# Kernel optimization log

Measured on AMD Instinct MI355X. Metric: run time of the kernel, lower is better.

The kernel has to match this reference:

```python
import jax, jax.numpy as jnp
import numpy as np

N, E = 100000, 1600000
IN, HID, HEADS, OUT = 128, 16, 8, 40
NEG_SLOPE = 0.2


def setup_inputs() -> dict:
    key = jax.random.key(0)
    ks = jax.random.split(key, 10)
    glorot = lambda k, shape, fan: (jax.random.normal(k, shape, jnp.float32) / np.float32(np.sqrt(fan)))
    return {
        "x": jax.random.normal(ks[0], (N, IN), jnp.float32),
        "edge_index": jax.random.randint(ks[1], (2, E), 0, N, dtype=jnp.int64),
        "W1": glorot(ks[2], (IN, HEADS * HID), IN),
        "att_src1": glorot(ks[3], (HEADS, HID), HID),
        "att_dst1": glorot(ks[4], (HEADS, HID), HID),
        "b1": jnp.zeros((HEADS * HID,), jnp.float32),
        "W2": glorot(ks[5], (HEADS * HID, OUT), HEADS * HID),
        "att_src2": glorot(ks[6], (1, OUT), OUT),
        "att_dst2": glorot(ks[7], (1, OUT), OUT),
        "b2": jnp.zeros((OUT,), jnp.float32),
    }


def gat_conv(x, W, a_src, a_dst, b, src, dst, n, heads, ch, concat):
    # x: [n, in], W: [in, heads*ch]
    h = (x @ W).reshape(n, heads, ch)                      # [n, H, C]
    e_s = jnp.einsum("nhc,hc->nh", h, a_src)               # per-node src logits
    e_d = jnp.einsum("nhc,hc->nh", h, a_dst)               # per-node dst logits
    alpha = jax.nn.leaky_relu(e_s[src] + e_d[dst], NEG_SLOPE)  # [E, H]
    # numerically stable softmax over incoming edges of each dst node
    m = jax.lax.stop_gradient(jax.ops.segment_max(alpha, dst, num_segments=n))
    ex = jnp.exp(alpha - m[dst])
    denom = jax.ops.segment_sum(ex, dst, num_segments=n)
    a = ex / (denom[dst] + 1e-16)                          # [E, H]
    out = jax.ops.segment_sum(h[src] * a[:, :, None], dst, num_segments=n)  # [n, H, C]
    out = out.reshape(n, heads * ch) if concat else out.mean(axis=1)
    return out + b


def reference(x, edge_index, W1, att_src1, att_dst1, b1, W2, att_src2, att_dst2, b2):
    n = x.shape[0]
    loops = jnp.arange(n, dtype=edge_index.dtype)
    src = jnp.concatenate([edge_index[0], loops])  # add_self_loops (PyG default)
    dst = jnp.concatenate([edge_index[1], loops])
    h1 = jax.nn.relu(gat_conv(x, W1, att_src1, att_dst1, b1, src, dst, n, HEADS, HID, True))
    # F.dropout(training=False) is identity in inference
    h2 = gat_conv(h1, W2, att_src2, att_dst2, b2, src, dst, n, 1, OUT, False)
    return jax.nn.log_softmax(h2, axis=1)
```

## Files before the change

### kernel.cpp

```cpp
#include <hip/hip_runtime.h>
#include <hip/hip_fp16.h>
#include <math.h>

#define NN 100000
#define EE 1600000
#define ET (EE + NN)
#define BWN 64
#define NBUCK 1563
#define ACHUNK 4096
#define NAB 416
#define MAXS 1792

typedef _Float16 f16x8 __attribute__((ext_vector_type(8)));
typedef float f32x4 __attribute__((ext_vector_type(4)));
typedef float f32x2 __attribute__((ext_vector_type(2)));

__device__ __forceinline__ float lrelu(float x) { return x > 0.f ? x : 0.2f * x; }

__global__ void k_w1pack(const float* __restrict__ W1, __half* __restrict__ w1p) {
    int idx = blockIdx.x * 256 + threadIdx.x;
    int j = idx & 7, lane = (idx >> 3) & 63, k0 = (idx >> 9) & 3;
    int ct = (idx >> 11) & 7;
    int k = k0 * 32 + (lane >> 4) * 8 + j;
    int c = ct * 16 + (lane & 15);
    _Float16 v = (_Float16)W1[k * 128 + c];
    w1p[idx] = *(__half*)&v;
}

__global__ void k_w2pack(const float* __restrict__ W2, __half* __restrict__ w2p) {
    int idx = blockIdx.x * 256 + threadIdx.x;
    int j = idx & 7, lane = (idx >> 3) & 63, k0 = (idx >> 9) & 3;
    int ct = idx >> 11;
    int k = k0 * 32 + (lane >> 4) * 8 + j;
    int c = ct * 16 + (lane & 15);
    _Float16 v = (_Float16)((c < 40) ? W2[k * 40 + c] : 0.f);
    w2p[idx] = *(__half*)&v;
}

__global__ __launch_bounds__(256) void k_gemm1(
        const float* __restrict__ x, const __half* __restrict__ w1p,
        const float* __restrict__ as1, const float* __restrict__ ad1,
        unsigned* __restrict__ h1b, float* __restrict__ es1, float* __restrict__ ed1) {
    int tid = threadIdx.x;
    int w = tid >> 6, lane = tid & 63;
    int rb = blockIdx.x * 64 + w * 16;
    int l15 = lane & 15, rg = lane >> 4;

    int arow = rb + l15;
    bool aok = arow < NN;
    const float4* x4 = (const float4*)x;
    f16x8 ah[4];
    #pragma unroll
    for (int k0 = 0; k0 < 4; ++k0) {
        float4 p0 = make_float4(0.f, 0.f, 0.f, 0.f), p1 = p0;
        if (aok) {
            int fi = arow * 32 + k0 * 8 + rg * 2;
            p0 = x4[fi];
            p1 = x4[fi + 1];
        }
        float pv[8] = {p0.x, p0.y, p0.z, p0.w, p1.x, p1.y, p1.z, p1.w};
        #pragma unroll
        for (int j = 0; j < 8; ++j) ah[k0][j] = (_Float16)pv[j];
    }

    const f16x8* w1f = (const f16x8*)w1p;
    f32x4 acc[8];
    #pragma unroll
    for (int ct = 0; ct < 8; ++ct) acc[ct] = (f32x4){0.f, 0.f, 0.f, 0.f};
    #pragma unroll
    for (int ct = 0; ct < 8; ++ct) {
        #pragma unroll
        for (int k0 = 0; k0 < 4; ++k0) {
            f16x8 bh = w1f[(ct * 4 + k0) * 64 + lane];
            acc[ct] = __builtin_amdgcn_mfma_f32_16x16x32_f16(bh, ah[k0], acc[ct], 0, 0, 0);
        }
    }

    int row = rb + l15;
    bool rok = row < NN;
    #pragma unroll
    for (int ct = 0; ct < 8; ++ct) {
        if (rok) {
            unsigned pw = __builtin_amdgcn_cvt_pk_fp8_f32(acc[ct][0], acc[ct][1], 0u, false);
            pw = __builtin_amdgcn_cvt_pk_fp8_f32(acc[ct][2], acc[ct][3], pw, true);
            h1b[row * 32 + ct * 4 + rg] = pw;
        }
        float4 a4 = ((const float4*)as1)[ct * 4 + rg];
        float4 d4 = ((const float4*)ad1)[ct * 4 + rg];
        float s = acc[ct][0] * a4.x + acc[ct][1] * a4.y + acc[ct][2] * a4.z + acc[ct][3] * a4.w;
        float d = acc[ct][0] * d4.x + acc[ct][1] * d4.y + acc[ct][2] * d4.z + acc[ct][3] * d4.w;
        s += __shfl_xor(s, 16); s += __shfl_xor(s, 32);
        d += __shfl_xor(d, 16); d += __shfl_xor(d, 32);
        if (rg == 0 && rok) { es1[row * 8 + ct] = s; ed1[row * 8 + ct] = d; }
    }
}

__global__ void k_bhist(const int* __restrict__ dst, int* __restrict__ bcnt) {
    __shared__ int lh[NBUCK];
    int t = threadIdx.x;
    for (int i = t; i < NBUCK; i += 256) lh[i] = 0;
    __syncthreads();
    int c0 = blockIdx.x * ACHUNK;
    #pragma unroll
    for (int i = 0; i < 16; ++i) {
        int e = c0 + t + i * 256;
        if (e < ET) {
            int d = (e < EE) ? dst[e] : e - EE;
            atomicAdd(&lh[d >> 6], 1);
        }
    }
    __syncthreads();
    for (int i = t; i < NBUCK; i += 256) {
        int c = lh[i];
        if (c) atomicAdd(&bcnt[i], c);
    }
}

__global__ void k_bscan(const int* __restrict__ bcnt, int* __restrict__ bbase,
                        int* __restrict__ bcur) {
    __shared__ int sd[256];
    int t = threadIdx.x;
    int base = t * 8;
    int v[8];
    int s = 0;
    #pragma unroll
    for (int j = 0; j < 8; ++j) {
        int i = base + j;
        v[j] = (i < NBUCK) ? bcnt[i] : 0;
        s += v[j];
    }
    sd[t] = s;
    __syncthreads();
    for (int off = 1; off < 256; off <<= 1) {
        int x = (t >= off) ? sd[t - off] : 0;
        __syncthreads();
        sd[t] += x;
        __syncthreads();
    }
    int excl = sd[t] - s;
    #pragma unroll
    for (int j = 0; j < 8; ++j) {
        int i = base + j;
        if (i <= NBUCK) { bbase[i] = excl; if (i < NBUCK) bcur[i] = excl; }
        excl += v[j];
    }
}

__global__ void k_bscatter(const int* __restrict__ src, const int* __restrict__ dst,
                           int* __restrict__ bcur, unsigned int* __restrict__ bedge) {
    __shared__ int lh[NBUCK];
    __shared__ int lb[NBUCK];
    int t = threadIdx.x;
    for (int i = t; i < NBUCK; i += 256) lh[i] = 0;
    __syncthreads();
    int c0 = blockIdx.x * ACHUNK;
    unsigned int val[16];
    int bkt[16];
    int rnk[16];
    #pragma unroll
    for (int i = 0; i < 16; ++i) {
        int e = c0 + t + i * 256;
        if (e < ET) {
            int s, d;
            if (e < EE) { s = src[e]; d = dst[e]; } else { s = d = e - EE; }
            int b = d >> 6;
            bkt[i] = b;
            val[i] = (unsigned)s | ((unsigned)(d & 63) << 24);
            rnk[i] = atomicAdd(&lh[b], 1);
        } else bkt[i] = -1;
    }
    __syncthreads();
    for (int i = t; i < NBUCK; i += 256) {
        int c = lh[i];
        lb[i] = c ? atomicAdd(&bcur[i], c) : 0;
    }
    __syncthreads();
    #pragma unroll
    for (int i = 0; i < 16; ++i)
        if (bkt[i] >= 0) bedge[lb[bkt[i]] + rnk[i]] = val[i];
}

__global__ void k_place(const unsigned int* __restrict__ bedge,
                        const int* __restrict__ bbase, int* __restrict__ rp,
                        int* __restrict__ col) {
    __shared__ int lh[BWN];
    __shared__ int ex[BWN + 1];
    __shared__ int lcur[BWN];
    __shared__ int stg[MAXS];
    int b = blockIdx.x, t = threadIdx.x;
    int beg = bbase[b], end = bbase[b + 1];
    if (t < BWN) { lh[t] = 0; lcur[t] = 0; }
    __syncthreads();
    for (int e = beg + t; e < end; e += 256) atomicAdd(&lh[(bedge[e] >> 24) & 63], 1);
    __syncthreads();
    if (t < 64) {
        int v = lh[t];
        int x = v;
        #pragma unroll
        for (int off = 1; off < 64; off <<= 1) {
            int y = __shfl_up(x, off);
            if (t >= off) x += y;
        }
        ex[t] = x - v;
        if (t == 63) ex[64] = x;
    }
    __syncthreads();
    int n = b * BWN + t;
    if (t < BWN && n < NN) rp[n] = beg + ex[t];
    if (b == 0 && t == 0) rp[NN] = ET;
    int S = ex[BWN];
    int lane = t & 63, w = t >> 6;
    if (S <= MAXS) {
        for (int e = beg + t; e < end; e += 256) {
            unsigned u = bedge[e];
            int i = (u >> 24) & 63;
            int pos = ex[i] + atomicAdd(&lcur[i], 1);
            stg[pos] = (int)(u & 0xFFFFFFu);
        }
        __syncthreads();
        for (int i = w; i < BWN; i += 4) {
            int sb = ex[i], d = lh[i];
            if (d <= 1) continue;
            if (d <= 64) {
                int vv = (lane < d) ? stg[sb + lane] : 0x7fffffff;
                #pragma unroll
                for (int k = 2; k <= 64; k <<= 1) {
                    #pragma unroll
                    for (int j = k >> 1; j > 0; j >>= 1) {
                        int other = __shfl_xor(vv, j);
                        bool lower = (lane & j) == 0;
                        bool up = (lane & k) == 0;
                        vv = (lower == up) ? min(vv, other) : max(vv, other);
                    }
                }
                if (lane < d) stg[sb + lane] = vv;
            } else if (lane == 0) {
                for (int p = sb + 1; p < sb + d; ++p) {
                    int key = stg[p]; int j = p - 1;
                    while (j >= sb && stg[j] > key) { stg[j + 1] = stg[j]; --j; }
                    stg[j + 1] = key;
                }
            }
        }
        __syncthreads();
        for (int j = t; j < S; j += 256) col[beg + j] = stg[j];
    } else {
        for (int e = beg + t; e < end; e += 256) {
            unsigned u = bedge[e];
            int i = (u >> 24) & 63;
            int pos = beg + ex[i] + atomicAdd(&lcur[i], 1);
            col[pos] = (int)(u & 0xFFFFFFu);
        }
        __syncthreads();
        if (t < BWN) {
            int sb = beg + ex[t], d = lh[t];
            for (int p = sb + 1; p < sb + d; ++p) {
                int key = col[p]; int j = p - 1;
                while (j >= sb && col[j] > key) { col[j + 1] = col[j]; --j; }
                col[j + 1] = key;
            }
        }
    }
}

__global__ void k_agg1(const int* __restrict__ rp, const int* __restrict__ col,
                       const uint4* __restrict__ h1v, const float* __restrict__ es1,
                       const float* __restrict__ ed1, const float* __restrict__ b1,
                       __half* __restrict__ out1h) {
    int gid = blockIdx.x * blockDim.x + threadIdx.x;
    int n = gid >> 3;
    int l = threadIdx.x & 7;
    if (n >= NN) return;
    float edn = ed1[n * 8 + l];
    int beg = rp[n], end = rp[n + 1];
    float acc[16];
    #pragma unroll
    for (int j = 0; j < 16; ++j) acc[j] = 0.f;
    float den = 0.f;
    int e = beg;
    int sA = col[e];
    int eB = (e + 1 < end) ? e + 1 : e;
    int sB = col[eB];
    float esA = es1[sA * 8 + l], esB = es1[sB * 8 + l];
    uint4 uA = h1v[sA * 8 + l];
    uint4 uB = h1v[sB * 8 + l];
    while (e < end) {
        int en = e + 2;
        int enA = (en < end) ? en : e;
        int enB = (en + 1 < end) ? en + 1 : enA;
        int nsA = col[enA], nsB = col[enB];
        float nesA = es1[nsA * 8 + l], nesB = es1[nsB * 8 + l];
        uint4 nuA = h1v[nsA * 8 + l];
        uint4 nuB = h1v[nsB * 8 + l];
        float exA = __expf(lrelu(esA + edn));
        float exB = (e + 1 < end) ? __expf(lrelu(esB + edn)) : 0.f;
        den += exA;
        den += exB;
        const unsigned* wA = (const unsigned*)&uA;
        const unsigned* wB = (const unsigned*)&uB;
        #pragma unroll
        for (int j = 0; j < 4; ++j) {
            f32x2 a01 = __builtin_amdgcn_cvt_pk_f32_fp8(wA[j], false);
            f32x2 a23 = __builtin_amdgcn_cvt_pk_f32_fp8(wA[j], true);
            f32x2 b01 = __builtin_amdgcn_cvt_pk_f32_fp8(wB[j], false);
            f32x2 b23 = __builtin_amdgcn_cvt_pk_f32_fp8(wB[j], true);
            acc[j * 4 + 0] += exA * a01.x; acc[j * 4 + 0] += exB * b01.x;
            acc[j * 4 + 1] += exA * a01.y; acc[j * 4 + 1] += exB * b01.y;
            acc[j * 4 + 2] += exA * a23.x; acc[j * 4 + 2] += exB * b23.x;
            acc[j * 4 + 3] += exA * a23.y; acc[j * 4 + 3] += exB * b23.y;
        }
        e = en;
        esA = nesA; esB = nesB;
        uA = nuA; uB = nuB;
    }
    float inv = 1.f / (den + 1e-16f);
    union { __half2 h[8]; uint4 u[2]; } cv;
    #pragma unroll
    for (int i = 0; i < 4; ++i) {
        float4 b = ((const float4*)b1)[l * 4 + i];
        float o0 = fmaxf(acc[i * 4]     * inv + b.x, 0.f);
        float o1 = fmaxf(acc[i * 4 + 1] * inv + b.y, 0.f);
        float o2 = fmaxf(acc[i * 4 + 2] * inv + b.z, 0.f);
        float o3 = fmaxf(acc[i * 4 + 3] * inv + b.w, 0.f);
        cv.h[i * 2]     = __floats2half2_rn(o0, o1);
        cv.h[i * 2 + 1] = __floats2half2_rn(o2, o3);
    }
    ((uint4*)out1h)[n * 16 + l * 2]     = cv.u[0];
    ((uint4*)out1h)[n * 16 + l * 2 + 1] = cv.u[1];
}

__global__ __launch_bounds__(256) void k_gemm2(
        const __half* __restrict__ out1h, const __half* __restrict__ w2p,
        const float* __restrict__ as2, const float* __restrict__ ad2,
        __half* __restrict__ h2h, float* __restrict__ es2, float* __restrict__ ed2) {
    int tid = threadIdx.x;
    int w = tid >> 6, lane = tid & 63;
    int rb = blockIdx.x * 64 + w * 16;
    int l15 = lane & 15, rg = lane >> 4;

    int arow = rb + l15;
    bool aok = arow < NN;
    f16x8 af[4];
    #pragma unroll
    for (int k0 = 0; k0 < 4; ++k0) {
        uint4 u = make_uint4(0, 0, 0, 0);
        if (aok) u = ((const uint4*)out1h)[arow * 16 + k0 * 4 + rg];
        af[k0] = *(f16x8*)&u;
    }

    const f16x8* w2f = (const f16x8*)w2p;
    int row = rb + l15;
    bool rok = row < NN;
    float sacc = 0.f, dacc = 0.f;
    #pragma unroll
    for (int ct = 0; ct < 3; ++ct) {
        f32x4 acc = (f32x4){0.f, 0.f, 0.f, 0.f};
        #pragma unroll
        for (int k0 = 0; k0 < 4; ++k0) {
            f16x8 bh = w2f[(ct * 4 + k0) * 64 + lane];
            acc = __builtin_amdgcn_mfma_f32_16x16x32_f16(bh, af[k0], acc, 0, 0, 0);
        }
        int cbase = ct * 16 + rg * 4;
        if (cbase < 40) {
            float4 a4 = ((const float4*)as2)[ct * 4 + rg];
            float4 d4 = ((const float4*)ad2)[ct * 4 + rg];
            sacc += acc[0] * a4.x + acc[1] * a4.y + acc[2] * a4.z + acc[3] * a4.w;
            dacc += acc[0] * d4.x + acc[1] * d4.y + acc[2] * d4.z + acc[3] * d4.w;
            if (rok) {
                union { __half2 h[2]; uint2 u; } cv;
                cv.h[0] = __floats2half2_rn(acc[0], acc[1]);
                cv.h[1] = __floats2half2_rn(acc[2], acc[3]);
                *(uint2*)&h2h[row * 40 + cbase] = cv.u;
            }
        }
    }
    sacc += __shfl_xor(sacc, 16); sacc += __shfl_xor(sacc, 32);
    dacc += __shfl_xor(dacc, 16); dacc += __shfl_xor(dacc, 32);
    if (rg == 0 && rok) { es2[row] = sacc; ed2[row] = dacc; }
}

__global__ void k_agg2(const int* __restrict__ rp, const int* __restrict__ col,
                       const uint4* __restrict__ h2v, const float* __restrict__ es2,
                       const float* __restrict__ ed2, const float* __restrict__ b2,
                       float* __restrict__ out) {
    int gid = blockIdx.x * blockDim.x + threadIdx.x;
    int n = gid >> 3;
    int l = threadIdx.x & 7;
    if (n >= NN) return;
    bool qv = l < 5;
    float edn = ed2[n];
    int beg = rp[n], end = rp[n + 1];
    float acc[8];
    #pragma unroll
    for (int j = 0; j < 8; ++j) acc[j] = 0.f;
    float den = 0.f;
    int e = beg;
    int sA = col[e];
    int eB = (e + 1 < end) ? e + 1 : e;
    int sB = col[eB];
    float esA = es2[sA], esB = es2[sB];
    uint4 uA = qv ? h2v[sA * 5 + l] : make_uint4(0, 0, 0, 0);
    uint4 uB = qv ? h2v[sB * 5 + l] : make_uint4(0, 0, 0, 0);
    while (e < end) {
        int en = e + 2;
        int enA = (en < end) ? en : e;
        int enB = (en + 1 < end) ? en + 1 : enA;
        int nsA = col[enA], nsB = col[enB];
        float nesA = es2[nsA], nesB = es2[nsB];
        uint4 nuA = qv ? h2v[nsA * 5 + l] : make_uint4(0, 0, 0, 0);
        uint4 nuB = qv ? h2v[nsB * 5 + l] : make_uint4(0, 0, 0, 0);
        float exA = __expf(lrelu(esA + edn));
        float exB = (e + 1 < end) ? __expf(lrelu(esB + edn)) : 0.f;
        den += exA;
        den += exB;
        const __half2* pA = (const __half2*)&uA;
        const __half2* pB = (const __half2*)&uB;
        #pragma unroll
        for (int j = 0; j < 4; ++j) {
            float2 fA = __half22float2(pA[j]);
            float2 fB = __half22float2(pB[j]);
            acc[j * 2]     += exA * fA.x; acc[j * 2]     += exB * fB.x;
            acc[j * 2 + 1] += exA * fA.y; acc[j * 2 + 1] += exB * fB.y;
        }
        e = en;
        esA = nesA; esB = nesB;
        uA = nuA; uB = nuB;
    }
    float inv = 1.f / (den + 1e-16f);
    float v[8];
    float m = -INFINITY;
    if (qv) {
        #pragma unroll
        for (int j = 0; j < 8; ++j) {
            v[j] = acc[j] * inv + b2[l * 8 + j];
            m = fmaxf(m, v[j]);
        }
    }
    #pragma unroll
    for (int o = 1; o <= 4; o <<= 1) m = fmaxf(m, __shfl_xor(m, o));
    float es = 0.f;
    if (qv) {
        #pragma unroll
        for (int j = 0; j < 8; ++j) es += __expf(v[j] - m);
    }
    #pragma unroll
    for (int o = 1; o <= 4; o <<= 1) es += __shfl_xor(es, o);
    if (qv) {
        float ls = m + __logf(es);
        float4 o0, o1;
        o0.x = v[0] - ls; o0.y = v[1] - ls; o0.z = v[2] - ls; o0.w = v[3] - ls;
        o1.x = v[4] - ls; o1.y = v[5] - ls; o1.z = v[6] - ls; o1.w = v[7] - ls;
        ((float4*)out)[n * 10 + l * 2]     = o0;
        ((float4*)out)[n * 10 + l * 2 + 1] = o1;
    }
}

extern "C" void kernel_launch(void* const* d_in, const int* in_sizes, int n_in,
                              void* d_out, int out_size, void* d_ws, size_t ws_size,
                              hipStream_t stream) {
    const float* x   = (const float*)d_in[0];
    const int*   ei  = (const int*)d_in[1];
    const float* W1  = (const float*)d_in[2];
    const float* as1 = (const float*)d_in[3];
    const float* ad1 = (const float*)d_in[4];
    const float* b1  = (const float*)d_in[5];
    const float* W2  = (const float*)d_in[6];
    const float* as2 = (const float*)d_in[7];
    const float* ad2 = (const float*)d_in[8];
    const float* b2  = (const float*)d_in[9];
    float* out = (float*)d_out;

    const int* esrc = ei;
    const int* edst = ei + EE;

    unsigned* h1b = (unsigned*)d_ws;
    float* es1  = (float*)(h1b + NN * 32);
    float* ed1  = es1 + NN * 8;
    __half* out1h = (__half*)(ed1 + NN * 8);
    __half* h2h = out1h + NN * 128;
    float* es2  = (float*)(h2h + NN * 40);
    float* ed2  = es2 + NN;
    int* rp     = (int*)(ed2 + NN);
    int* col    = rp + NN + 1;
    int* bcnt   = col + ET;
    int* bbase  = bcnt + NBUCK;
    int* bcur   = bbase + NBUCK + 1;
    unsigned int* bedge = (unsigned int*)(bcur + NBUCK);
    __half* w1p = (__half*)(bedge + ET);
    __half* w2p = w1p + 16384;

    hipMemsetAsync(bcnt, 0, NBUCK * sizeof(int), stream);
    k_bhist<<<NAB, 256, 0, stream>>>(edst, bcnt);
    k_bscan<<<1, 256, 0, stream>>>(bcnt, bbase, bcur);
    k_bscatter<<<NAB, 256, 0, stream>>>(esrc, edst, bcur, bedge);
    k_place<<<NBUCK, 256, 0, stream>>>(bedge, bbase, rp, col);

    k_w1pack<<<64, 256, 0, stream>>>(W1, w1p);
    k_gemm1<<<(NN + 63) / 64, 256, 0, stream>>>(x, w1p, as1, ad1, h1b, es1, ed1);
    k_agg1<<<(NN * 8 + 255) / 256, 256, 0, stream>>>(rp, col, (const uint4*)h1b, es1, ed1, b1, out1h);

    k_w2pack<<<24, 256, 0, stream>>>(W2, w2p);
    k_gemm2<<<(NN + 63) / 64, 256, 0, stream>>>(out1h, w2p, as2, ad2, h2h, es2, ed2);
    k_agg2<<<(NN * 8 + 255) / 256, 256, 0, stream>>>(rp, col, (const uint4*)h2h, es2, ed2, b2, out);
}
```

Baseline: 242.3 us.

## Fuse layer-2 projection and attention logits into layer-1 aggregation kernel

Folds the layer-2 linear transform (out1 @ W2) and the es2/ed2 logit computation into the epilogue of the layer-1 aggregation. Each group of 8 lanes multiplies its 16 ReLU outputs against W2 staged in LDS, then reduces the 40 partial sums across lanes with shuffles. This removes the out1h intermediate write and read, plus the w2pack and gemm2 launches. In exchange it replaces MFMA with scalar FMAs and 120 shuffles per lane, adds per-block LDS loading of W2 (about 20 KB), and raises register pressure with a 40-float array, which may lower occupancy of the latency-bound gather loop.

```diff
diff --git a/kernel.cpp b/kernel.cpp
--- a/kernel.cpp
+++ b/kernel.cpp
@@ -25,16 +25,6 @@
     int c = ct * 16 + (lane & 15);
     _Float16 v = (_Float16)W1[k * 128 + c];
     w1p[idx] = *(__half*)&v;
-}
-
-__global__ void k_w2pack(const float* __restrict__ W2, __half* __restrict__ w2p) {
-    int idx = blockIdx.x * 256 + threadIdx.x;
-    int j = idx & 7, lane = (idx >> 3) & 63, k0 = (idx >> 9) & 3;
-    int ct = idx >> 11;
-    int k = k0 * 32 + (lane >> 4) * 8 + j;
-    int c = ct * 16 + (lane & 15);
-    _Float16 v = (_Float16)((c < 40) ? W2[k * 40 + c] : 0.f);
-    w2p[idx] = *(__half*)&v;
 }
 
 __global__ __launch_bounds__(256) void k_gemm1(
@@ -263,14 +253,23 @@
     }
 }
 
-__global__ void k_agg1(const int* __restrict__ rp, const int* __restrict__ col,
-                       const uint4* __restrict__ h1v, const float* __restrict__ es1,
-                       const float* __restrict__ ed1, const float* __restrict__ b1,
-                       __half* __restrict__ out1h) {
-    int gid = blockIdx.x * blockDim.x + threadIdx.x;
+__global__ __launch_bounds__(256) void k_agg1(
+        const int* __restrict__ rp, const int* __restrict__ col,
+        const uint4* __restrict__ h1v, const float* __restrict__ es1,
+        const float* __restrict__ ed1, const float* __restrict__ b1,
+        const float* __restrict__ W2, const float* __restrict__ as2,
+        const float* __restrict__ ad2, __half* __restrict__ h2h,
+        float* __restrict__ es2, float* __restrict__ ed2) {
+    __shared__ float w2s[128 * 41];
+    int tid = threadIdx.x;
+    for (int i = tid; i < 128 * 40; i += 256) {
+        int k = i / 40, c = i - k * 40;
+        w2s[k * 41 + c] = W2[i];
+    }
+    __syncthreads();
+    int gid = blockIdx.x * 256 + tid;
     int n = gid >> 3;
-    int l = threadIdx.x & 7;
-    if (n >= NN) return;
+    int l = tid & 7;
     float edn = ed1[n * 8 + l];
     int beg = rp[n], end = rp[n + 1];
     float acc[16];
@@ -314,69 +313,41 @@
         uA = nuA; uB = nuB;
     }
     float inv = 1.f / (den + 1e-16f);
-    union { __half2 h[8]; uint4 u[2]; } cv;
+    float row[16];
     #pragma unroll
     for (int i = 0; i < 4; ++i) {
         float4 b = ((const float4*)b1)[l * 4 + i];
-        float o0 = fmaxf(acc[i * 4]     * inv + b.x, 0.f);
-        float o1 = fmaxf(acc[i * 4 + 1] * inv + b.y, 0.f);
-        float o2 = fmaxf(acc[i * 4 + 2] * inv + b.z, 0.f);
-        float o3 = fmaxf(acc[i * 4 + 3] * inv + b.w, 0.f);
-        cv.h[i * 2]     = __floats2half2_rn(o0, o1);
-        cv.h[i * 2 + 1] = __floats2half2_rn(o2, o3);
-    }
-    ((uint4*)out1h)[n * 16 + l * 2]     = cv.u[0];
-    ((uint4*)out1h)[n * 16 + l * 2 + 1] = cv.u[1];
-}
-
-__global__ __launch_bounds__(256) void k_gemm2(
-        const __half* __restrict__ out1h, const __half* __restrict__ w2p,
-        const float* __restrict__ as2, const float* __restrict__ ad2,
-        __half* __restrict__ h2h, float* __restrict__ es2, float* __restrict__ ed2) {
-    int tid = threadIdx.x;
-    int w = tid >> 6, lane = tid & 63;
-    int rb = blockIdx.x * 64 + w * 16;
-    int l15 = lane & 15, rg = lane >> 4;
-
-    int arow = rb + l15;
-    bool aok = arow < NN;
-    f16x8 af[4];
-    #pragma unroll
-    for (int k0 = 0; k0 < 4; ++k0) {
-        uint4 u = make_uint4(0, 0, 0, 0);
-        if (aok) u = ((const uint4*)out1h)[arow * 16 + k0 * 4 + rg];
-        af[k0] = *(f16x8*)&u;
-    }
-
-    const f16x8* w2f = (const f16x8*)w2p;
-    int row = rb + l15;
-    bool rok = row < NN;
-    float sacc = 0.f, dacc = 0.f;
-    #pragma unroll
-    for (int ct = 0; ct < 3; ++ct) {
-        f32x4 acc = (f32x4){0.f, 0.f, 0.f, 0.f};
-        #pragma unroll
-        for (int k0 = 0; k0 < 4; ++k0) {
-            f16x8 bh = w2f[(ct * 4 + k0) * 64 + lane];
-            acc = __builtin_amdgcn_mfma_f32_16x16x32_f16(bh, af[k0], acc, 0, 0, 0);
-        }
-        int cbase = ct * 16 + rg * 4;
-        if (cbase < 40) {
-            float4 a4 = ((const float4*)as2)[ct * 4 + rg];
-            float4 d4 = ((const float4*)ad2)[ct * 4 + rg];
-            sacc += acc[0] * a4.x + acc[1] * a4.y + acc[2] * a4.z + acc[3] * a4.w;
-            dacc += acc[0] * d4.x + acc[1] * d4.y + acc[2] * d4.z + acc[3] * d4.w;
-            if (rok) {
-                union { __half2 h[2]; uint2 u; } cv;
-                cv.h[0] = __floats2half2_rn(acc[0], acc[1]);
-                cv.h[1] = __floats2half2_rn(acc[2], acc[3]);
-                *(uint2*)&h2h[row * 40 + cbase] = cv.u;
-            }
-        }
-    }
-    sacc += __shfl_xor(sacc, 16); sacc += __shfl_xor(sacc, 32);
-    dacc += __shfl_xor(dacc, 16); dacc += __shfl_xor(dacc, 32);
-    if (rg == 0 && rok) { es2[row] = sacc; ed2[row] = dacc; }
+        row[i * 4 + 0] = fmaxf(acc[i * 4 + 0] * inv + b.x, 0.f);
+        row[i * 4 + 1] = fmaxf(acc[i * 4 + 1] * inv + b.y, 0.f);
+        row[i * 4 + 2] = fmaxf(acc[i * 4 + 2] * inv + b.z, 0.f);
+        row[i * 4 + 3] = fmaxf(acc[i * 4 + 3] * inv + b.w, 0.f);
+    }
+    float p[40];
+    #pragma unroll
+    for (int c = 0; c < 40; ++c) p[c] = 0.f;
+    #pragma unroll
+    for (int j = 0; j < 16; ++j) {
+        float rv = row[j];
+        const float* wr = &w2s[(l * 16 + j) * 41];
+        #pragma unroll
+        for (int c = 0; c < 40; ++c) p[c] += rv * wr[c];
+    }
+    #pragma unroll
+    for (int o = 1; o <= 4; o <<= 1) {
+        #pragma unroll
+        for (int c = 0; c < 40; ++c) p[c] += __shfl_xor(p[c], o);
+    }
+    float s = 0.f, d = 0.f;
+    #pragma unroll
+    for (int c = 0; c < 40; ++c) { s += p[c] * as2[c]; d += p[c] * ad2[c]; }
+    if (l == 0) { es2[n] = s; ed2[n] = d; }
+    if (l < 5) {
+        union { __half2 h[4]; uint4 u; } cv;
+        #pragma unroll
+        for (int i = 0; i < 4; ++i)
+            cv.h[i] = __floats2half2_rn(p[l * 8 + i * 2], p[l * 8 + i * 2 + 1]);
+        ((uint4*)h2h)[n * 5 + l] = cv.u;
+    }
 }
 
 __global__ void k_agg2(const int* __restrict__ rp, const int* __restrict__ col,
@@ -476,8 +447,7 @@
     unsigned* h1b = (unsigned*)d_ws;
     float* es1  = (float*)(h1b + NN * 32);
     float* ed1  = es1 + NN * 8;
-    __half* out1h = (__half*)(ed1 + NN * 8);
-    __half* h2h = out1h + NN * 128;
+    __half* h2h = (__half*)(ed1 + NN * 8);
     float* es2  = (float*)(h2h + NN * 40);
     float* ed2  = es2 + NN;
     int* rp     = (int*)(ed2 + NN);
@@ -487,7 +457,6 @@
     int* bcur   = bbase + NBUCK + 1;
     unsigned int* bedge = (unsigned int*)(bcur + NBUCK);
     __half* w1p = (__half*)(bedge + ET);
-    __half* w2p = w1p + 16384;
 
     hipMemsetAsync(bcnt, 0, NBUCK * sizeof(int), stream);
     k_bhist<<<NAB, 256, 0, stream>>>(edst, bcnt);
@@ -497,9 +466,9 @@
 
     k_w1pack<<<64, 256, 0, stream>>>(W1, w1p);
     k_gemm1<<<(NN + 63) / 64, 256, 0, stream>>>(x, w1p, as1, ad1, h1b, es1, ed1);
-    k_agg1<<<(NN * 8 + 255) / 256, 256, 0, stream>>>(rp, col, (const uint4*)h1b, es1, ed1, b1, out1h);
-
-    k_w2pack<<<24, 256, 0, stream>>>(W2, w2p);
-    k_gemm2<<<(NN + 63) / 64, 256, 0, stream>>>(out1h, w2p, as2, ad2, h2h, es2, ed2);
+
+    k_agg1<<<(NN * 8) / 256, 256, 0, stream>>>(rp, col, (const uint4*)h1b, es1, ed1,
+                                               b1, W2, as2, ad2, h2h, es2, ed2);
+
     k_agg2<<<(NN * 8 + 255) / 256, 256, 0, stream>>>(rp, col, (const uint4*)h2h, es2, ed2, b2, out);
 }
```

New measurement: 318.9 us. +31.6%, slower.
